# Performance work log

Hardware: AMD Instinct MI355X
Metric: run time of the kernel (lower is better)

The kernel has to match this reference:

```python
import jax, jax.numpy as jnp
import numpy as np

# COCO person skeleton: 19 limbs over 17 keypoints (matches COCO_PERSON_SKELETON)
SKELETON = np.array([(15,13),(13,11),(16,14),(14,12),(11,12),(5,11),(6,12),(5,6),
                     (5,7),(6,8),(7,9),(8,10),(1,2),(0,1),(0,2),(1,3),(2,4),(3,5),(4,6)], dtype=np.int32)
P = 20              # max peaks kept per keypoint (fixed-shape stand-in for argwhere)
S = 10              # line-integral samples (np.linspace(..., 10) in original)
PEAK_THRESH = 0.1
PAF_SCORE_THRESH = 0.05
PAF_COUNT_THRESH = 0.8


def setup_inputs() -> dict:
    key = jax.random.key(0)
    k1, k2 = jax.random.split(key)
    B, K, H, W = 32, 17, 192, 192
    C = SKELETON.shape[0]
    heat_pred = jax.random.uniform(k1, (B, K, H, W), dtype=jnp.float32)
    paf_pred = jax.random.normal(k2, (B, 2 * C, H, W), dtype=jnp.float32) * 0.5
    return {"heat_pred": heat_pred, "paf_pred": paf_pred}


def reference(heat_pred, paf_pred):
    heat, paf = heat_pred, paf_pred
    B, K, H, W = heat.shape
    C = SKELETON.shape[0]

    # ---- 3x3 local-maxima NMS (== scipy maximum_filter(size=3) comparison) ----
    mx = jax.lax.reduce_window(heat, -jnp.inf, jax.lax.max, (1, 1, 3, 3), (1, 1, 1, 1), "SAME")
    peak_mask = (heat == mx) & (heat > PEAK_THRESH)

    # ---- sub-pixel quadratic refinement (interior pixels only) ----
    right = jnp.pad(heat[..., 1:], ((0, 0), (0, 0), (0, 0), (0, 1)))
    left = jnp.pad(heat[..., :-1], ((0, 0), (0, 0), (0, 0), (1, 0)))
    down = jnp.pad(heat[..., 1:, :], ((0, 0), (0, 0), (0, 1), (0, 0)))
    up = jnp.pad(heat[..., :-1, :], ((0, 0), (0, 0), (1, 0), (0, 0)))
    dx = 0.5 * (right - left)
    dy = 0.5 * (down - up)
    dxx = right + left - 2.0 * heat
    dyy = down + up - 2.0 * heat
    dx = jnp.where(dxx != 0, dx / (-dxx), dx)
    dy = jnp.where(dyy != 0, dy / (-dyy), dy)
    xg = jnp.arange(W)
    yg = jnp.arange(H)
    interior = (((xg > 0) & (xg < W - 1))[None, :] & ((yg > 0) & (yg < H - 1))[:, None])
    dx = jnp.where(interior, dx, 0.0)
    dy = jnp.where(interior, dy, 0.0)

    # ---- fixed-size top-P peak extraction per (image, keypoint) ----
    score_m = jnp.where(peak_mask, heat, -1.0).reshape(B, K, H * W)
    top_s, top_i = jax.lax.top_k(score_m, P)               # [B,K,P]
    valid = top_s > PEAK_THRESH
    py = (top_i // W).astype(jnp.float32)
    px = (top_i % W).astype(jnp.float32)
    dxf = jnp.take_along_axis(dx.reshape(B, K, H * W), top_i, axis=2)
    dyf = jnp.take_along_axis(dy.reshape(B, K, H * W), top_i, axis=2)
    px = px + dxf
    py = py + dyf
    peaks = jnp.stack([px, py, top_s], axis=-1) * valid[..., None].astype(heat.dtype)  # [B,K,P,3]

    # ---- PAF line-integral association scores (all limbs vectorized) ----
    A = jnp.asarray(SKELETON[:, 0])
    Bi = jnp.asarray(SKELETON[:, 1])
    ax, ay, sa, va = px[:, A], py[:, A], top_s[:, A], valid[:, A]   # [B,C,P]
    bx, by, sb, vb = px[:, Bi], py[:, Bi], top_s[:, Bi], valid[:, Bi]
    dxl = bx[:, :, None, :] - ax[:, :, :, None]                      # [B,C,P,P]
    dyl = by[:, :, None, :] - ay[:, :, :, None]
    norm = jnp.sqrt(dxl * dxl + dyl * dyl) + 1e-8
    vx, vy = dxl / norm, dyl / norm
    t = jnp.linspace(0.0, 1.0, S)
    xs = ax[:, :, :, None, None] + dxl[..., None] * t                # [B,C,P,P,S]
    ys = ay[:, :, :, None, None] + dyl[..., None] * t
    xi = xs.astype(jnp.int32)   # truncation, same as np .astype(int)
    yi = ys.astype(jnp.int32)
    inb = (xi >= 0) & (xi < W) & (yi >= 0) & (yi < H)
    xi = jnp.clip(xi, 0, W - 1)
    yi = jnp.clip(yi, 0, H - 1)
    paf_x = paf[:, 0::2].reshape(B, C, H * W)
    paf_y = paf[:, 1::2].reshape(B, C, H * W)
    idxf = (yi * W + xi).reshape(B, C, -1)
    pxv = jnp.take_along_axis(paf_x, idxf, axis=2).reshape(B, C, P, P, S)
    pyv = jnp.take_along_axis(paf_y, idxf, axis=2).reshape(B, C, P, P, S)
    vs = pxv * vx[..., None] + pyv * vy[..., None]                   # dot with unit limb vector
    inbf = inb.astype(vs.dtype)
    cnt = inbf.sum(-1)
    mean_score = (vs * inbf).sum(-1) / jnp.maximum(cnt, 1.0)
    ratio = ((vs > PAF_SCORE_THRESH).astype(vs.dtype) * inbf).sum(-1) / jnp.maximum(cnt, 1.0)
    ok = (cnt > 0) & (mean_score > 0) & (ratio > PAF_COUNT_THRESH) & va[:, :, :, None] & vb[:, :, None, :]
    conn = jnp.where(ok, mean_score + 0.5 * (sa[:, :, :, None] + sb[:, :, None, :]), 0.0)  # [B,C,P,P]
    return peaks, conn
```

## Files before the change

### kernel.cpp

```cpp
#include <hip/hip_runtime.h>
#include <cstdint>

constexpr int Bn = 32, Kn = 17, Hn = 192, Wn = 192, Cn = 19, Pn = 20, Sn = 10;
constexpr int HWn = Hn * Wn;
constexpr int NSTRIP = 4, STRIPROWS = Hn / NSTRIP;
constexpr int PEAKS_FLOATS = Bn * Kn * Pn * 3;
constexpr int NPAIR = Pn * Pn;
constexpr int STK = 19;
constexpr int CH_ROWS = 48, CH_PIX = CH_ROWS * Wn;

__constant__ int d_SKA[Cn] = {15,13,16,14,11,5,6,5,5,6,7,8,1,0,0,1,2,3,4};
__constant__ int d_SKB[Cn] = {13,11,14,12,12,11,12,6,7,8,9,10,2,1,2,3,4,5,6};

__device__ __forceinline__ float m3(float a, float b, float c) {
    return fmaxf(fmaxf(a, b), c);
}

__global__ __launch_bounds__(256, 4) void topk_strip(const float* __restrict__ heat,
                                                     unsigned long long* __restrict__ strip_out) {
    const int img = blockIdx.x >> 2;
    const int strip = blockIdx.x & 3;
    const float* __restrict__ hp = heat + (size_t)img * HWn;
    const int tid = threadIdx.x;

    __shared__ unsigned long long stack[256 * STK];
    __shared__ unsigned long long wmax[4];
    const int sbase = tid * STK;
    int scnt = 0;

#pragma unroll 1
    for (int it = 0; it < 9; ++it) {
        const int q = it * 256 + tid;
        const int ry = q / 48;
        const int qx = q - ry * 48;
        const int gy = strip * STRIPROWS + ry;
        const int x0 = qx * 4;
        const float* rp = hp + gy * Wn + x0;

        const bool hl = x0 > 0, hr = x0 < Wn - 4;
        float4 cc = *(const float4*)rp;
        float cl = hl ? rp[-1] : -INFINITY;
        float cr = hr ? rp[4] : -INFINITY;

        float4 tt = make_float4(-INFINITY, -INFINITY, -INFINITY, -INFINITY);
        float tl = -INFINITY, tr = -INFINITY;
        if (gy > 0) {
            tt = *(const float4*)(rp - Wn);
            if (hl) tl = rp[-Wn - 1];
            if (hr) tr = rp[-Wn + 4];
        }
        float4 bb = make_float4(-INFINITY, -INFINITY, -INFINITY, -INFINITY);
        float bl = -INFINITY, br = -INFINITY;
        if (gy < Hn - 1) {
            bb = *(const float4*)(rp + Wn);
            if (hl) bl = rp[Wn - 1];
            if (hr) br = rp[Wn + 4];
        }

        float n0 = m3(m3(tl, tt.x, tt.y), m3(cl, cc.x, cc.y), m3(bl, bb.x, bb.y));
        float n1 = m3(m3(tt.x, tt.y, tt.z), m3(cc.x, cc.y, cc.z), m3(bb.x, bb.y, bb.z));
        float n2 = m3(m3(tt.y, tt.z, tt.w), m3(cc.y, cc.z, cc.w), m3(bb.y, bb.z, bb.w));
        float n3 = m3(m3(tt.z, tt.w, tr), m3(cc.z, cc.w, cr), m3(bb.z, bb.w, br));

        const int pidx = gy * Wn + x0;
#pragma unroll
        for (int i = 0; i < 4; ++i) {
            float v = (i == 0) ? cc.x : (i == 1) ? cc.y : (i == 2) ? cc.z : cc.w;
            float nm = (i == 0) ? n0 : (i == 1) ? n1 : (i == 2) ? n2 : n3;
            if (v > 0.1f && v >= nm && scnt < STK) {
                unsigned int u = __float_as_uint(v) | 0x80000000u;
                unsigned long long key = ((unsigned long long)u << 32) |
                                         (unsigned long long)(0xFFFFFFFFu - (unsigned)(pidx + i));
                stack[sbase + scnt] = key;
                ++scnt;
            }
        }
    }

    unsigned long long cand[Pn];
#pragma unroll
    for (int j = 0; j < Pn; ++j) cand[j] = 0ULL;
#pragma unroll 1
    for (int e = 0; e < scnt; ++e) {
        unsigned long long key = stack[sbase + e];
#pragma unroll
        for (int j = 0; j < Pn; ++j) {
            if (key > cand[j]) { unsigned long long t = cand[j]; cand[j] = key; key = t; }
        }
    }
    __syncthreads();

    const int lane = tid & 63, wid = tid >> 6;
    unsigned long long* out = strip_out + (size_t)blockIdx.x * Pn;

#pragma unroll 1
    for (int slot = 0; slot < Pn; ++slot) {
        unsigned long long r = cand[0];
#pragma unroll
        for (int o = 32; o > 0; o >>= 1) {
            unsigned long long other = __shfl_xor(r, o, 64);
            if (other > r) r = other;
        }
        if (lane == 0) wmax[wid] = r;
        __syncthreads();
        unsigned long long best = wmax[0];
        if (wmax[1] > best) best = wmax[1];
        if (wmax[2] > best) best = wmax[2];
        if (wmax[3] > best) best = wmax[3];
        __syncthreads();

        if (best != 0ULL && cand[0] == best) {
#pragma unroll
            for (int j = 0; j < Pn - 1; ++j) cand[j] = cand[j + 1];
            cand[Pn - 1] = 0ULL;
            out[slot] = best;
        }
        if (best == 0ULL && tid == 0) out[slot] = 0ULL;
    }
}

__global__ __launch_bounds__(64) void topk_merge(const float* __restrict__ heat,
                                                 const unsigned long long* __restrict__ strip_out,
                                                 float* __restrict__ out_peaks) {
    const int img = blockIdx.x;
    const int t = threadIdx.x;
    const unsigned long long* sp = strip_out + (size_t)img * (NSTRIP * Pn);
    unsigned long long key0 = sp[t];
    unsigned long long key1 = (t < NSTRIP * Pn - 64) ? sp[64 + t] : 0ULL;
    const float* __restrict__ hp = heat + (size_t)img * HWn;

#pragma unroll 1
    for (int slot = 0; slot < Pn; ++slot) {
        unsigned long long m = (key0 > key1) ? key0 : key1;
        unsigned long long r = m;
#pragma unroll
        for (int o = 32; o > 0; o >>= 1) {
            unsigned long long other = __shfl_xor(r, o, 64);
            if (other > r) r = other;
        }
        if (r != 0ULL && m == r) {
            if (key0 == r) { key0 = key1; key1 = 0ULL; } else { key1 = 0ULL; }
            unsigned int u = (unsigned int)(r >> 32);
            float v = __uint_as_float(u & 0x7FFFFFFFu);
            int idx = (int)(0xFFFFFFFFu - (unsigned int)(r & 0xFFFFFFFFu));
            int y = idx / Wn;
            int x = idx - y * Wn;
            float dx = 0.0f, dy = 0.0f;
            if (x >= 1 && x <= Wn - 2 && y >= 1 && y <= Hn - 2) {
                float rr = hp[idx + 1], ll = hp[idx - 1];
                float dd = hp[idx + Wn], uu = hp[idx - Wn];
                float dx0 = 0.5f * (rr - ll);
                float dxx = rr + ll - 2.0f * v;
                dx = (dxx != 0.0f) ? dx0 / (-dxx) : dx0;
                float dy0 = 0.5f * (dd - uu);
                float dyy = dd + uu - 2.0f * v;
                dy = (dyy != 0.0f) ? dy0 / (-dyy) : dy0;
            }
            float* o = out_peaks + ((size_t)img * Pn + slot) * 3;
            o[0] = (float)x + dx;
            o[1] = (float)y + dy;
            o[2] = v;
        }
        if (r == 0ULL && t == 0) {
            float* o = out_peaks + ((size_t)img * Pn + slot) * 3;
            o[0] = 0.0f; o[1] = 0.0f; o[2] = 0.0f;
        }
    }
}

__global__ __launch_bounds__(512, 2) void conn_staged(const float* __restrict__ paf,
                                                      const float* __restrict__ peaks,
                                                      float* __restrict__ conn) {
    __shared__ float sx[CH_PIX];
    __shared__ float sy[CH_PIX];
    const int bc = blockIdx.x;
    const int b = bc / Cn;
    const int c = bc - b * Cn;
    const int tid = threadIdx.x;
    const float* __restrict__ pafx = paf + (size_t)(b * (2 * Cn) + 2 * c) * HWn;
    const float* __restrict__ pafy = pafx + HWn;

    const bool act = tid < NPAIR;
    float vx = 0.0f, vy = 0.0f, sa = 0.0f, sb = 0.0f;
    int sidx[Sn];
    bool sin_[Sn];
    if (act) {
        const int i = tid / Pn, j = tid - (tid / Pn) * Pn;
        const int ka = d_SKA[c], kb = d_SKB[c];
        const float* pa = peaks + ((size_t)(b * Kn + ka) * Pn + i) * 3;
        const float* pb = peaks + ((size_t)(b * Kn + kb) * Pn + j) * 3;
        float ax = pa[0], ay = pa[1];
        sa = pa[2];
        float bx = pb[0], by = pb[1];
        sb = pb[2];
        float dxl = bx - ax, dyl = by - ay;
        float norm = sqrtf(dxl * dxl + dyl * dyl) + 1e-8f;
        vx = dxl / norm;
        vy = dyl / norm;
#pragma unroll
        for (int s = 0; s < Sn; ++s) {
            float t = (s == Sn - 1) ? 1.0f : (float)s * (1.0f / 9.0f);
            float xs = ax + dxl * t;
            float ys = ay + dyl * t;
            int xi = (int)xs;
            int yi = (int)ys;
            sin_[s] = (xi >= 0) && (xi < Wn) && (yi >= 0) && (yi < Hn);
            int xc = min(max(xi, 0), Wn - 1);
            int yc = min(max(yi, 0), Hn - 1);
            sidx[s] = yc * Wn + xc;
        }
    } else {
#pragma unroll
        for (int s = 0; s < Sn; ++s) { sidx[s] = 0; sin_[s] = false; }
    }

    float sum = 0.0f;
    int cnt = 0, pos = 0;
#pragma unroll 1
    for (int ch = 0; ch < Hn / CH_ROWS; ++ch) {
        const int r0 = ch * CH_PIX;
        const float4* gx = (const float4*)(pafx + r0);
        const float4* gy = (const float4*)(pafy + r0);
        float4* lx = (float4*)sx;
        float4* ly = (float4*)sy;
        for (int k = tid; k < CH_PIX / 4; k += 512) {
            lx[k] = gx[k];
            ly[k] = gy[k];
        }
        __syncthreads();
        if (act) {
#pragma unroll
            for (int s = 0; s < Sn; ++s) {
                int rel = sidx[s] - r0;
                if (sin_[s] && rel >= 0 && rel < CH_PIX) {
                    float vs = sx[rel] * vx + sy[rel] * vy;
                    ++cnt;
                    sum += vs;
                    if (vs > 0.05f) ++pos;
                }
            }
        }
        __syncthreads();
    }

    if (act) {
        float denom = fmaxf((float)cnt, 1.0f);
        float mean = sum / denom;
        float ratio = (float)pos / denom;
        bool ok = (cnt > 0) && (mean > 0.0f) && (ratio > 0.8f) && (sa > 0.1f) && (sb > 0.1f);
        conn[(size_t)bc * NPAIR + tid] = ok ? (mean + 0.5f * (sa + sb)) : 0.0f;
    }
}

extern "C" void kernel_launch(void* const* d_in, const int* in_sizes, int n_in,
                              void* d_out, int out_size, void* d_ws, size_t ws_size,
                              hipStream_t stream) {
    const float* heat = (const float*)d_in[0];
    const float* paf  = (const float*)d_in[1];
    float* out   = (float*)d_out;
    float* peaks = out;
    float* conn  = out + PEAKS_FLOATS;
    unsigned long long* strips = (unsigned long long*)d_ws;

    topk_strip<<<Bn * Kn * NSTRIP, 256, 0, stream>>>(heat, strips);
    topk_merge<<<Bn * Kn, 64, 0, stream>>>(heat, strips, peaks);
    conn_staged<<<Bn * Cn, 512, 0, stream>>>(paf, peaks, conn);
}
```

Measured before the change: 389.0 us.

## Replace per-thread insertion sort with per-wave top-k extraction and smaller PAF chunks

The strip kernel drops the per-thread 20-entry insertion sort and the block-wide barriers. Each thread now tracks its running maximum candidate, and each wave extracts its own top-20 by repeated shuffle reduction, rescanning only the winning thread's small stack. The merge kernel now combines 16 wave lists per image instead of 4 strip lists, and defers the sub-pixel refinement so 20 lanes compute it in parallel. The connection kernel uses 32-row chunks, so less shared memory lets 3 blocks fit per CU, and it replaces the in-bounds flags with a sentinel index and an unsigned range check. The costs are 4x more workspace traffic and a serial rescan in the strip kernel.

Result: faster. 367.5 us (-5.5%).

```diff
diff --git a/kernel.cpp b/kernel.cpp
--- a/kernel.cpp
+++ b/kernel.cpp
@@ -7,7 +7,8 @@
 constexpr int PEAKS_FLOATS = Bn * Kn * Pn * 3;
 constexpr int NPAIR = Pn * Pn;
 constexpr int STK = 19;
-constexpr int CH_ROWS = 48, CH_PIX = CH_ROWS * Wn;
+constexpr int CH_ROWS = 32, CH_PIX = CH_ROWS * Wn;
+constexpr int NCH = Hn / CH_ROWS;
 
 __constant__ int d_SKA[Cn] = {15,13,16,14,11,5,6,5,5,6,7,8,1,0,0,1,2,3,4};
 __constant__ int d_SKB[Cn] = {13,11,14,12,12,11,12,6,7,8,9,10,2,1,2,3,4,5,6};
@@ -17,16 +18,17 @@
 }
 
 __global__ __launch_bounds__(256, 4) void topk_strip(const float* __restrict__ heat,
-                                                     unsigned long long* __restrict__ strip_out) {
+                                                     unsigned long long* __restrict__ wave_out) {
     const int img = blockIdx.x >> 2;
     const int strip = blockIdx.x & 3;
     const float* __restrict__ hp = heat + (size_t)img * HWn;
     const int tid = threadIdx.x;
 
     __shared__ unsigned long long stack[256 * STK];
-    __shared__ unsigned long long wmax[4];
     const int sbase = tid * STK;
     int scnt = 0;
+    unsigned long long cmax = 0ULL;
+    int cpos = 0;
 
 #pragma unroll 1
     for (int it = 0; it < 9; ++it) {
@@ -72,77 +74,81 @@
                 unsigned long long key = ((unsigned long long)u << 32) |
                                          (unsigned long long)(0xFFFFFFFFu - (unsigned)(pidx + i));
                 stack[sbase + scnt] = key;
+                if (key > cmax) { cmax = key; cpos = scnt; }
                 ++scnt;
             }
         }
     }
 
-    unsigned long long cand[Pn];
-#pragma unroll
-    for (int j = 0; j < Pn; ++j) cand[j] = 0ULL;
-#pragma unroll 1
-    for (int e = 0; e < scnt; ++e) {
-        unsigned long long key = stack[sbase + e];
-#pragma unroll
-        for (int j = 0; j < Pn; ++j) {
-            if (key > cand[j]) { unsigned long long t = cand[j]; cand[j] = key; key = t; }
-        }
-    }
-    __syncthreads();
-
     const int lane = tid & 63, wid = tid >> 6;
-    unsigned long long* out = strip_out + (size_t)blockIdx.x * Pn;
+    unsigned long long* out = wave_out + ((size_t)blockIdx.x * 4 + wid) * Pn;
 
 #pragma unroll 1
     for (int slot = 0; slot < Pn; ++slot) {
-        unsigned long long r = cand[0];
+        unsigned long long r = cmax;
 #pragma unroll
         for (int o = 32; o > 0; o >>= 1) {
-            unsigned long long other = __shfl_xor(r, o, 64);
-            if (other > r) r = other;
-        }
-        if (lane == 0) wmax[wid] = r;
-        __syncthreads();
-        unsigned long long best = wmax[0];
-        if (wmax[1] > best) best = wmax[1];
-        if (wmax[2] > best) best = wmax[2];
-        if (wmax[3] > best) best = wmax[3];
-        __syncthreads();
-
-        if (best != 0ULL && cand[0] == best) {
-#pragma unroll
-            for (int j = 0; j < Pn - 1; ++j) cand[j] = cand[j + 1];
-            cand[Pn - 1] = 0ULL;
-            out[slot] = best;
-        }
-        if (best == 0ULL && tid == 0) out[slot] = 0ULL;
+            unsigned long long t = __shfl_xor(r, o, 64);
+            if (t > r) r = t;
+        }
+        if (r != 0ULL && cmax == r) {
+            --scnt;
+            stack[sbase + cpos] = stack[sbase + scnt];
+            cmax = 0ULL; cpos = 0;
+            for (int e = 0; e < scnt; ++e) {
+                unsigned long long k2 = stack[sbase + e];
+                if (k2 > cmax) { cmax = k2; cpos = e; }
+            }
+        }
+        if (lane == 0) out[slot] = r;
     }
 }
 
 __global__ __launch_bounds__(64) void topk_merge(const float* __restrict__ heat,
-                                                 const unsigned long long* __restrict__ strip_out,
+                                                 const unsigned long long* __restrict__ wave_out,
                                                  float* __restrict__ out_peaks) {
     const int img = blockIdx.x;
     const int t = threadIdx.x;
-    const unsigned long long* sp = strip_out + (size_t)img * (NSTRIP * Pn);
-    unsigned long long key0 = sp[t];
-    unsigned long long key1 = (t < NSTRIP * Pn - 64) ? sp[64 + t] : 0ULL;
+    const unsigned long long* sp = wave_out + (size_t)img * (NSTRIP * 4 * Pn);
+    unsigned long long k0 = sp[t];
+    unsigned long long k1 = sp[t + 64];
+    unsigned long long k2 = sp[t + 128];
+    unsigned long long k3 = sp[t + 192];
+    unsigned long long k4 = sp[t + 256];
     const float* __restrict__ hp = heat + (size_t)img * HWn;
 
+    unsigned long long mine = 0ULL;
 #pragma unroll 1
     for (int slot = 0; slot < Pn; ++slot) {
-        unsigned long long m = (key0 > key1) ? key0 : key1;
+        unsigned long long m = k0;
+        if (k1 > m) m = k1;
+        if (k2 > m) m = k2;
+        if (k3 > m) m = k3;
+        if (k4 > m) m = k4;
         unsigned long long r = m;
 #pragma unroll
         for (int o = 32; o > 0; o >>= 1) {
-            unsigned long long other = __shfl_xor(r, o, 64);
-            if (other > r) r = other;
+            unsigned long long x = __shfl_xor(r, o, 64);
+            if (x > r) r = x;
         }
         if (r != 0ULL && m == r) {
-            if (key0 == r) { key0 = key1; key1 = 0ULL; } else { key1 = 0ULL; }
-            unsigned int u = (unsigned int)(r >> 32);
+            if (k0 == r)      { k0 = k1; k1 = k2; k2 = k3; k3 = k4; k4 = 0ULL; }
+            else if (k1 == r) { k1 = k2; k2 = k3; k3 = k4; k4 = 0ULL; }
+            else if (k2 == r) { k2 = k3; k3 = k4; k4 = 0ULL; }
+            else if (k3 == r) { k3 = k4; k4 = 0ULL; }
+            else              { k4 = 0ULL; }
+        }
+        if (t == slot) mine = r;
+    }
+
+    if (t < Pn) {
+        float* o = out_peaks + ((size_t)img * Pn + t) * 3;
+        if (mine == 0ULL) {
+            o[0] = 0.0f; o[1] = 0.0f; o[2] = 0.0f;
+        } else {
+            unsigned int u = (unsigned int)(mine >> 32);
             float v = __uint_as_float(u & 0x7FFFFFFFu);
-            int idx = (int)(0xFFFFFFFFu - (unsigned int)(r & 0xFFFFFFFFu));
+            int idx = (int)(0xFFFFFFFFu - (unsigned int)(mine & 0xFFFFFFFFu));
             int y = idx / Wn;
             int x = idx - y * Wn;
             float dx = 0.0f, dy = 0.0f;
@@ -156,19 +162,14 @@
                 float dyy = dd + uu - 2.0f * v;
                 dy = (dyy != 0.0f) ? dy0 / (-dyy) : dy0;
             }
-            float* o = out_peaks + ((size_t)img * Pn + slot) * 3;
             o[0] = (float)x + dx;
             o[1] = (float)y + dy;
             o[2] = v;
         }
-        if (r == 0ULL && t == 0) {
-            float* o = out_peaks + ((size_t)img * Pn + slot) * 3;
-            o[0] = 0.0f; o[1] = 0.0f; o[2] = 0.0f;
-        }
-    }
-}
-
-__global__ __launch_bounds__(512, 2) void conn_staged(const float* __restrict__ paf,
+    }
+}
+
+__global__ __launch_bounds__(512, 3) void conn_staged(const float* __restrict__ paf,
                                                       const float* __restrict__ peaks,
                                                       float* __restrict__ conn) {
     __shared__ float sx[CH_PIX];
@@ -182,8 +183,8 @@
 
     const bool act = tid < NPAIR;
     float vx = 0.0f, vy = 0.0f, sa = 0.0f, sb = 0.0f;
+    int cnt = 0;
     int sidx[Sn];
-    bool sin_[Sn];
     if (act) {
         const int i = tid / Pn, j = tid - (tid / Pn) * Pn;
         const int ka = d_SKA[c], kb = d_SKB[c];
@@ -204,40 +205,41 @@
             float ys = ay + dyl * t;
             int xi = (int)xs;
             int yi = (int)ys;
-            sin_[s] = (xi >= 0) && (xi < Wn) && (yi >= 0) && (yi < Hn);
-            int xc = min(max(xi, 0), Wn - 1);
-            int yc = min(max(yi, 0), Hn - 1);
-            sidx[s] = yc * Wn + xc;
+            bool inb = (xi >= 0) && (xi < Wn) && (yi >= 0) && (yi < Hn);
+            if (inb) {
+                ++cnt;
+                sidx[s] = yi * Wn + xi;
+            } else {
+                sidx[s] = -0x40000000;
+            }
         }
     } else {
 #pragma unroll
-        for (int s = 0; s < Sn; ++s) { sidx[s] = 0; sin_[s] = false; }
+        for (int s = 0; s < Sn; ++s) sidx[s] = -0x40000000;
     }
 
     float sum = 0.0f;
-    int cnt = 0, pos = 0;
-#pragma unroll 1
-    for (int ch = 0; ch < Hn / CH_ROWS; ++ch) {
+    int pos = 0;
+#pragma unroll 1
+    for (int ch = 0; ch < NCH; ++ch) {
         const int r0 = ch * CH_PIX;
         const float4* gx = (const float4*)(pafx + r0);
         const float4* gy = (const float4*)(pafy + r0);
         float4* lx = (float4*)sx;
         float4* ly = (float4*)sy;
-        for (int k = tid; k < CH_PIX / 4; k += 512) {
-            lx[k] = gx[k];
-            ly[k] = gy[k];
+#pragma unroll
+        for (int k = 0; k < CH_PIX / 4 / 512; ++k) {
+            lx[k * 512 + tid] = gx[k * 512 + tid];
+            ly[k * 512 + tid] = gy[k * 512 + tid];
         }
         __syncthreads();
-        if (act) {
-#pragma unroll
-            for (int s = 0; s < Sn; ++s) {
-                int rel = sidx[s] - r0;
-                if (sin_[s] && rel >= 0 && rel < CH_PIX) {
-                    float vs = sx[rel] * vx + sy[rel] * vy;
-                    ++cnt;
-                    sum += vs;
-                    if (vs > 0.05f) ++pos;
-                }
+#pragma unroll
+        for (int s = 0; s < Sn; ++s) {
+            unsigned rel = (unsigned)(sidx[s] - r0);
+            if (rel < (unsigned)CH_PIX) {
+                float vs = sx[rel] * vx + sy[rel] * vy;
+                sum += vs;
+                if (vs > 0.05f) ++pos;
             }
         }
         __syncthreads();
@@ -260,9 +262,9 @@
     float* out   = (float*)d_out;
     float* peaks = out;
     float* conn  = out + PEAKS_FLOATS;
-    unsigned long long* strips = (unsigned long long*)d_ws;
-
-    topk_strip<<<Bn * Kn * NSTRIP, 256, 0, stream>>>(heat, strips);
-    topk_merge<<<Bn * Kn, 64, 0, stream>>>(heat, strips, peaks);
+    unsigned long long* waves = (unsigned long long*)d_ws;
+
+    topk_strip<<<Bn * Kn * NSTRIP, 256, 0, stream>>>(heat, waves);
+    topk_merge<<<Bn * Kn, 64, 0, stream>>>(heat, waves, peaks);
     conn_staged<<<Bn * Cn, 512, 0, stream>>>(paf, peaks, conn);
 }
```
